# Kernel optimization log

Hardware: AMD Instinct MI355X
Metric: run time of the kernel (lower is better)

## Reference

```python
import jax, jax.numpy as jnp
import numpy as np

B, N, DIM, H, DH, K = 4, 2048, 512, 6, 64, 16
KEEP_PROB = 0.9  # 1 - dropout_rate
LOG2PI = float(np.log(2.0 * np.pi))
LOG_PRIOR = float(np.log(1.0 / K))


def setup_inputs() -> dict:
    key = jax.random.key(0)
    ks = jax.random.split(key, 7)
    inputs_q = jax.random.normal(ks[0], (B, N, DIM), dtype=jnp.float32)
    # decoder-style causal mask, shape [B, 1, q_len, kv_len]
    causal = jnp.tril(jnp.ones((N, N), dtype=jnp.float32))
    mask = jnp.broadcast_to(causal[None, None], (B, 1, N, N))
    # dropout keep mask broadcast across the query dim: [B, H, 1, kv_len]
    keep = jax.random.bernoulli(ks[1], KEEP_PROB, (B, H, 1, N)).astype(jnp.float32)
    w_qkv = jax.random.normal(ks[2], (DIM, 3 * H * DH), dtype=jnp.float32) * 0.02
    w_out = jax.random.normal(ks[3], (H * DH, DIM), dtype=jnp.float32) * 0.02
    mu_lookup = jax.random.normal(ks[4], (K, DIM), dtype=jnp.float32)
    logvar_lookup = jax.random.normal(ks[5], (K, DIM), dtype=jnp.float32) * 0.1
    return {
        "inputs_q": inputs_q,
        "mask": mask,
        "keep": keep,
        "w_qkv": w_qkv,
        "w_out": w_out,
        "mu_lookup": mu_lookup,
        "logvar_lookup": logvar_lookup,
    }


def reference(inputs_q, mask, keep, w_qkv, w_out, mu_lookup, logvar_lookup):
    # --- MultiHeadDotProductAttention (self-attn path) ---
    qkv = (inputs_q @ w_qkv).reshape(B, N, 3, H, DH)  # [B,N,3,H,DH]
    q, k, v = qkv[:, :, 0], qkv[:, :, 1], qkv[:, :, 2]
    # bias: 0 where mask > 0, -1e10 elsewhere (note: no 1/sqrt(d) scaling, as in source)
    bias = jnp.where(mask > 0, 0.0, -1e10)
    attn_weights = jnp.einsum('bqhd,bkhd->bhqk', q, k) + bias  # [B,H,N,N]
    attn_weights = jax.nn.softmax(attn_weights, axis=-1)
    # broadcast dropout: mask shared across the query dim
    attn_weights = attn_weights * keep / KEEP_PROB
    attn_out = jnp.einsum('bhqk,bkhd->bqhd', attn_weights, v)
    attn_out = attn_out.reshape(B, N, H * DH) @ w_out  # [B,N,DIM]

    # --- GMM posterior approx q(y|x) ~= p(y|z) (approx_qy_x, vectorized over k) ---
    z = attn_out.mean(axis=1)  # pooled latent, [B,DIM]
    diff = z[:, None, :] - mu_lookup[None]  # [B,K,DIM]
    llh = -0.5 * jnp.sum(
        diff * diff / jnp.exp(logvar_lookup)[None] + logvar_lookup[None] + LOG2PI,
        axis=-1,
    )  # [B,K]
    logLogit_qy_x = llh + LOG_PRIOR
    qy_x = jax.nn.softmax(logLogit_qy_x, axis=1)  # [B,K]

    # combine mixture mean back in so both branches are live in one output
    return attn_out + (qy_x @ mu_lookup)[:, None, :]
```

## Files before the change

### kernel.cpp

```cpp
#include <hip/hip_runtime.h>
#include <cstdint>
#include <cstddef>

#define NH 6
#define NSEQ 2048
#define DIMD 512
#define BATCH 4
#define HD 384
#define LOG2PI_F 1.8378770664093453f
#define LOG2E_F 1.4426950408889634f
#define M12L2_F (-17.312340490667562f)

typedef __attribute__((ext_vector_type(8))) short short8;
typedef __attribute__((ext_vector_type(8))) unsigned short ushort8;
typedef __attribute__((ext_vector_type(4))) unsigned short ushort4v;
typedef __attribute__((ext_vector_type(4))) float floatx4;

__device__ inline unsigned short f2bf(float f){
  unsigned int u = __float_as_uint(f);
  u += 0x7FFFu + ((u>>16)&1u);
  return (unsigned short)(u>>16);
}

__device__ inline float exp2_raw(float x){
  float r; asm("v_exp_f32 %0, %1" : "=v"(r) : "v"(x)); return r;
}

#define GLD16(gp, lp) __builtin_amdgcn_global_load_lds( \
  (const __attribute__((address_space(1))) void*)(gp), \
  (__attribute__((address_space(3))) void*)(lp), 16, 0, 0)

__device__ inline void wtrans_body(
    const float* __restrict__ src, unsigned short* __restrict__ dst,
    int R, int C, int bx, int by, unsigned short* Ls, int t)
{
  const int r = t>>2, c0 = (t&3)*16;
  const int d0 = by*64, n0 = bx*64;
  #pragma unroll
  for (int j=0;j<16;j+=4){
    floatx4 v = *(const floatx4*)(src + (size_t)(d0+r)*C + n0 + c0 + j);
    #pragma unroll
    for(int jj=0;jj<4;jj++) Ls[r*72 + c0+j+jj] = f2bf(v[jj]);
  }
  __syncthreads();
  #pragma unroll
  for (int j=0;j<16;j+=8){
    ushort8 o;
    #pragma unroll
    for(int jj=0;jj<8;jj++) o[jj] = Ls[(c0+j+jj)*72 + r];
    *(ushort8*)(dst + (size_t)(n0+r)*R + d0 + c0 + j) = o;
  }
}

__global__ __launch_bounds__(256) void prep(
    const float* __restrict__ xq, unsigned short* __restrict__ xbf,
    const float* __restrict__ w_qkv, unsigned short* __restrict__ wqT,
    const float* __restrict__ w_out, unsigned short* __restrict__ woT)
{
  __shared__ __attribute__((aligned(16))) unsigned short Ls[64*72];
  const int bid = blockIdx.x, t = threadIdx.x;
  if (bid < 4096){
    int i = bid*256 + t;
    floatx4 v = *(const floatx4*)(xq + (size_t)i*4);
    ushort4v r;
    #pragma unroll
    for(int j=0;j<4;j++) r[j] = f2bf(v[j]);
    *(ushort4v*)(xbf + (size_t)i*4) = r;
  } else if (bid < 4240){
    int rb = bid - 4096;
    wtrans_body(w_qkv, wqT, 512, 1152, rb%18, rb/18, Ls, t);
  } else {
    int rb = bid - 4240;
    wtrans_body(w_out, woT, 384, 512, rb%8, rb/8, Ls, t);
  }
}

__global__ __launch_bounds__(256) void gemm_qkv(
    const unsigned short* __restrict__ A,
    const unsigned short* __restrict__ Bt,
    const float* __restrict__ keep,
    unsigned short* __restrict__ Qo, unsigned short* __restrict__ Ko,
    unsigned short* __restrict__ Vt)
{
  __shared__ __attribute__((aligned(16))) unsigned short Cs[128*132];
  unsigned short* As = Cs;
  unsigned short* Bs = Cs + 128*64;
  const int tid = threadIdx.x;
  const int w = tid>>6, lane = tid&63;
  const int wr = w>>1, wc = w&1;
  const int quad = lane>>4, l16 = lane&15;
  const int tM = blockIdx.x*128, tN = blockIdx.y*128;
  const int r8 = lane>>3, c8 = (lane&7)*8;
  floatx4 acc[4][4];
  floatx4 zed = {0.f,0.f,0.f,0.f};
  #pragma unroll
  for (int i=0;i<4;i++)
    #pragma unroll
    for(int j=0;j<4;j++) acc[i][j] = zed;

  for (int k0=0; k0<512; k0+=64){
    #pragma unroll
    for (int i=0;i<4;i++){
      int row = w*32 + i*8;
      GLD16(A  + (size_t)(tM+row+r8)*512 + k0 + c8, As + row*64);
      GLD16(Bt + (size_t)(tN+row+r8)*512 + k0 + c8, Bs + row*64);
    }
    __syncthreads();
    #pragma unroll
    for (int kk=0; kk<64; kk+=32){
      short8 af[4], bf[4];
      #pragma unroll
      for(int mt=0;mt<4;mt++)
        af[mt] = *(const short8*)(As + (wr*64+mt*16+l16)*64 + kk + quad*8);
      #pragma unroll
      for(int nt=0;nt<4;nt++)
        bf[nt] = *(const short8*)(Bs + (wc*64+nt*16+l16)*64 + kk + quad*8);
      #pragma unroll
      for(int mt=0;mt<4;mt++)
        #pragma unroll
        for(int nt=0;nt<4;nt++)
          acc[mt][nt] = __builtin_amdgcn_mfma_f32_16x16x32_bf16(af[mt], bf[nt], acc[mt][nt], 0,0,0);
    }
    __syncthreads();
  }
  #pragma unroll
  for(int mt=0;mt<4;mt++)
    #pragma unroll
    for(int nt=0;nt<4;nt++){
      int gcol = tN + wc*64 + nt*16 + l16;
      float qs = (gcol < 384) ? LOG2E_F : 1.0f;
      #pragma unroll
      for(int r=0;r<4;r++)
        Cs[(wr*64+mt*16+quad*4+r)*132 + wc*64+nt*16+l16] = f2bf(acc[mt][nt][r]*qs);
    }
  __syncthreads();
  if (blockIdx.y < 6){
    const int row = tid>>1, colh = (tid&1)*64;
    const int gcol0 = tN + colh;
    const int t = gcol0/384, rem = gcol0 - t*384, h = rem>>6;
    const int grow = tM + row, b = grow>>11, n = grow & 2047;
    unsigned short* dst = (t==0 ? Qo : Ko) + ((size_t)((b*NH+h)*NSEQ+n))*64;
    #pragma unroll
    for(int j=0;j<8;j++)
      *(ushort8*)(dst + j*8) = *(const ushort8*)(Cs + row*132 + colh + j*8);
  } else {
    const int dcol = tid>>1;
    const int nh   = (tid&1)*64;
    const int gcol = tN + dcol;
    const int rem = gcol - 768, h = rem>>6, dh = rem&63;
    const int b = tM>>11, nb = tM & 2047;
    const float* kp = keep + (size_t)(b*NH+h)*NSEQ + nb + nh;
    unsigned short* dst = Vt + ((size_t)((b*NH+h)*64 + dh))*NSEQ + nb + nh;
    #pragma unroll
    for (int j8=0;j8<8;j8++){
      floatx4 k0 = *(const floatx4*)(kp + j8*8);
      floatx4 k1 = *(const floatx4*)(kp + j8*8 + 4);
      ushort8 o;
      #pragma unroll
      for(int u=0;u<4;u++)
        o[u]   = (k0[u] < 0.5f) ? (unsigned short)0 : Cs[(nh + j8*8 + u)*132 + dcol];
      #pragma unroll
      for(int u=0;u<4;u++)
        o[4+u] = (k1[u] < 0.5f) ? (unsigned short)0 : Cs[(nh + j8*8 + 4 + u)*132 + dcol];
      *(ushort8*)(dst + j8*8) = o;
    }
  }
}

__global__ __launch_bounds__(256, 3) void attn_kernel(
    const unsigned short* __restrict__ Qg, const unsigned short* __restrict__ Kg,
    const unsigned short* __restrict__ VtG,
    unsigned short* __restrict__ atp,
    float* __restrict__ zpart)
{
  __shared__ __attribute__((aligned(16))) float sm[4*32*34 + 128];
  float* Ocs  = sm;
  float* accs = sm + 4*32*34;
  const int tid = threadIdx.x;
  const int w = tid>>6, lane = tid&63;
  const int quad = lane>>4, l16 = lane&15;
  const int bid = blockIdx.x;
  const int idx = bid>>3;
  const int bh  = (bid&7) + 8*(idx % 3);
  const int c   = 63 - idx/3;
  const int b = bh/NH, h = bh - b*NH;
  const unsigned short* Qb = Qg  + (size_t)bh*NSEQ*64;
  const int q0 = c*32;
  const int nkt = (c>>1) + 1;
  const int q_abs0 = q0 + l16;

  const unsigned short* Kl = Kg  + (size_t)bh*NSEQ*64 + (size_t)l16*64 + quad*8;
  const unsigned short* Vl = VtG + (size_t)bh*64*NSEQ + (size_t)l16*NSEQ + quad*8;

  short8 qf[2][2];
  #pragma unroll
  for(int mt=0;mt<2;mt++)
    #pragma unroll
    for(int kc=0;kc<2;kc++)
      qf[mt][kc] = *(const short8*)(Qb + (size_t)(q0+mt*16+l16)*64 + kc*32 + quad*8);

  floatx4 O[2][4];
  float accl[2] = {0.f, 0.f};
  floatx4 zed = {0.f,0.f,0.f,0.f};
  floatx4 m12v = {M12L2_F, M12L2_F, M12L2_F, M12L2_F};
  #pragma unroll
  for(int mt=0;mt<2;mt++)
    #pragma unroll
    for(int dt=0;dt<4;dt++) O[mt][dt] = zed;

  for (int kt = w; kt < nkt; kt += 4){
    const int kB = kt*64;
    short8 vf[2][4];
    const unsigned short* vp0 = Vl + kB;
    #pragma unroll
    for(int kh=0;kh<2;kh++)
      #pragma unroll
      for(int dt=0;dt<4;dt++)
        vf[kh][dt] = *(const short8*)(vp0 + (size_t)dt*32768 + kh*32);

    floatx4 sacc[2][4];
    #pragma unroll
    for(int mt=0;mt<2;mt++)
      #pragma unroll
      for(int nt=0;nt<4;nt++) sacc[mt][nt] = m12v;
    const unsigned short* kp0 = Kl + (size_t)kt*4096;
    #pragma unroll
    for(int nt=0;nt<4;nt++){
      short8 kf0 = *(const short8*)(kp0 + nt*1024);
      short8 kf1 = *(const short8*)(kp0 + nt*1024 + 32);
      #pragma unroll
      for(int mt=0;mt<2;mt++){
        sacc[mt][nt] = __builtin_amdgcn_mfma_f32_16x16x32_bf16(kf0, qf[mt][0], sacc[mt][nt], 0,0,0);
        sacc[mt][nt] = __builtin_amdgcn_mfma_f32_16x16x32_bf16(kf1, qf[mt][1], sacc[mt][nt], 0,0,0);
      }
    }

    const bool dia = (kt == nkt-1);
    #pragma unroll
    for(int mt=0;mt<2;mt++){
      const int qa = q_abs0 + mt*16;
      unsigned int d0[4], d1[4];
      float rs = 0.f;
      #pragma unroll
      for(int nt=0;nt<4;nt++){
        const int key0 = kB + nt*16 + quad*4;
        float p0 = exp2_raw(sacc[mt][nt][0]);
        float p1 = exp2_raw(sacc[mt][nt][1]);
        float p2 = exp2_raw(sacc[mt][nt][2]);
        float p3 = exp2_raw(sacc[mt][nt][3]);
        if (dia){
          p0 = (key0   <= qa) ? p0 : 0.f;
          p1 = (key0+1 <= qa) ? p1 : 0.f;
          p2 = (key0+2 <= qa) ? p2 : 0.f;
          p3 = (key0+3 <= qa) ? p3 : 0.f;
        }
        rs += (p0+p1) + (p2+p3);
        asm("v_cvt_pk_bf16_f32 %0, %1, %2" : "=v"(d0[nt]) : "v"(p0), "v"(p1));
        asm("v_cvt_pk_bf16_f32 %0, %1, %2" : "=v"(d1[nt]) : "v"(p2), "v"(p3));
      }
      accl[mt] += rs;
      #pragma unroll
      for(int kh=0;kh<2;kh++){
        unsigned int x0 = d0[2*kh],   x1 = d1[2*kh];
        unsigned int y0 = d0[2*kh+1], y1 = d1[2*kh+1];
        asm("v_permlane32_swap_b32 %0, %1" : "+v"(x0), "+v"(y0));
        asm("v_permlane16_swap_b32 %0, %1" : "+v"(x0), "+v"(y0));
        asm("v_permlane32_swap_b32 %0, %1" : "+v"(x1), "+v"(y1));
        asm("v_permlane16_swap_b32 %0, %1" : "+v"(x1), "+v"(y1));
        union { unsigned int u[4]; short8 s; } cvt;
        cvt.u[0] = x0; cvt.u[1] = x1; cvt.u[2] = y0; cvt.u[3] = y1;
        short8 pf = cvt.s;
        #pragma unroll
        for(int dt=0;dt<4;dt++)
          O[mt][dt] = __builtin_amdgcn_mfma_f32_16x16x32_bf16(pf, vf[kh][dt], O[mt][dt], 0,0,0);
      }
    }
  }

  #pragma unroll
  for(int mt=0;mt<2;mt++){
    accl[mt] += __shfl_xor(accl[mt], 16, 64);
    accl[mt] += __shfl_xor(accl[mt], 32, 64);
  }
  if (quad == 0){
    accs[w*32 + l16]      = accl[0];
    accs[w*32 + 16 + l16] = accl[1];
  }

  const int orow = tid>>3, oc4 = (tid&7)*4;
  float sc2 = 0.f;
  #pragma unroll
  for (int h2=0; h2<2; ++h2){
    float* Ow = Ocs + w*(32*34);
    #pragma unroll
    for(int mt=0;mt<2;mt++)
      #pragma unroll
      for(int d2=0;d2<2;d2++){
        const int dt = h2*2 + d2;
        #pragma unroll
        for(int r=0;r<4;r++)
          Ow[(mt*16+quad*4+r)*34 + d2*16 + l16] = O[mt][dt][r];
      }
    __syncthreads();
    if (h2 == 0){
      float as = accs[orow] + accs[32+orow] + accs[64+orow] + accs[96+orow];
      sc2 = (1.0f/0.9f) / as;
    }
    float fv[4];
    #pragma unroll
    for(int j=0;j<4;j++) fv[j] = 0.f;
    #pragma unroll
    for(int s=0;s<4;s++){
      const float* p = Ocs + s*(32*34) + orow*34 + oc4;
      #pragma unroll
      for(int j=0;j<4;j++) fv[j] += p[j];
    }
    ushort4v o4;
    #pragma unroll
    for(int j=0;j<4;j++){ fv[j] *= sc2; o4[j] = f2bf(fv[j]); }
    *(ushort4v*)(atp + ((size_t)(b*NSEQ + q0 + orow))*HD + h*64 + h2*32 + oc4) = o4;

    #pragma unroll
    for(int j=0;j<4;j++){
      fv[j] += __shfl_xor(fv[j], 8, 64);
      fv[j] += __shfl_xor(fv[j], 16, 64);
      fv[j] += __shfl_xor(fv[j], 32, 64);
    }
    if (lane < 8){
      floatx4 zv; zv[0]=fv[0]; zv[1]=fv[1]; zv[2]=fv[2]; zv[3]=fv[3];
      *(floatx4*)(zpart + ((size_t)(b*256 + c*4 + w))*384 + h*64 + h2*32 + lane*4) = zv;
    }
    __syncthreads();
  }
}

__global__ __launch_bounds__(256) void gmm_kernel(
    const float* __restrict__ zpart,
    const float* __restrict__ wo,
    const float* __restrict__ mu,
    const float* __restrict__ lv, float* __restrict__ c)
{
  __shared__ float zsl[384];
  __shared__ float zl[512];
  __shared__ float sh[16];
  __shared__ float qy[16];
  const int tid = threadIdx.x, b = blockIdx.x;
  for (int e = tid; e < 384; e += 256){
    const float* zp = zpart + (size_t)b*256*384 + e;
    float s0=0.f, s1=0.f, s2=0.f, s3=0.f;
    for (int i=0;i<256;i+=4){
      s0 += zp[(size_t)(i+0)*384];
      s1 += zp[(size_t)(i+1)*384];
      s2 += zp[(size_t)(i+2)*384];
      s3 += zp[(size_t)(i+3)*384];
    }
    zsl[e] = (s0+s1)+(s2+s3);
  }
  __syncthreads();
  #pragma unroll
  for(int dd=0;dd<2;dd++){
    const int d = tid + dd*256;
    float s = 0.f;
    for(int e=0;e<384;e++) s += zsl[e]*wo[(size_t)e*512+d];
    zl[d] = s*(1.0f/2048.0f);
  }
  __syncthreads();
  const int k = tid>>4, li = tid&15;
  float part = 0.f;
  for(int d=li; d<DIMD; d+=16){
    float m = mu[k*DIMD+d], l = lv[k*DIMD+d];
    float diff = zl[d] - m;
    part += diff*diff*__expf(-l) + l + LOG2PI_F;
  }
  #pragma unroll
  for(int off=8;off>=1;off>>=1) part += __shfl_xor(part, off, 64);
  if (li==0) sh[k] = part;
  __syncthreads();
  if (tid<16){
    float logit = -0.5f*sh[tid];
    float mx = logit;
    #pragma unroll
    for(int off=8;off>=1;off>>=1) mx = fmaxf(mx, __shfl_xor(mx, off, 64));
    float e = __expf(logit-mx);
    float se = e;
    #pragma unroll
    for(int off=8;off>=1;off>>=1) se += __shfl_xor(se, off, 64);
    qy[tid] = e/se;
  }
  __syncthreads();
  for(int d=tid; d<DIMD; d+=256){
    float accv = 0.f;
    #pragma unroll
    for(int kk=0;kk<16;kk++) accv += qy[kk]*mu[kk*DIMD+d];
    c[b*DIMD+d] = accv;
  }
}

__global__ __launch_bounds__(256) void gemm_proj(
    const unsigned short* __restrict__ A,
    const unsigned short* __restrict__ Bt,
    const float* __restrict__ cvec,
    float* __restrict__ out)
{
  __shared__ __attribute__((aligned(16))) unsigned short As[128*64];
  __shared__ __attribute__((aligned(16))) unsigned short Bs[128*64];
  const int tid = threadIdx.x;
  const int w = tid>>6, lane = tid&63;
  const int wr = w>>1, wc = w&1;
  const int quad = lane>>4, l16 = lane&15;
  const int tM = blockIdx.x*128, tN = blockIdx.y*128;
  const int r8 = lane>>3, c8 = (lane&7)*8;
  floatx4 acc[4][4];
  floatx4 zed = {0.f,0.f,0.f,0.f};
  #pragma unroll
  for (int i=0;i<4;i++)
    #pragma unroll
    for(int j=0;j<4;j++) acc[i][j] = zed;

  for (int k0=0; k0<384; k0+=64){
    #pragma unroll
    for (int i=0;i<4;i++){
      int row = w*32 + i*8;
      GLD16(A  + (size_t)(tM+row+r8)*384 + k0 + c8, As + row*64);
      GLD16(Bt + (size_t)(tN+row+r8)*384 + k0 + c8, Bs + row*64);
    }
    __syncthreads();
    #pragma unroll
    for (int kk=0; kk<64; kk+=32){
      short8 af[4], bf[4];
      #pragma unroll
      for(int mt=0;mt<4;mt++)
        af[mt] = *(const short8*)(As + (wr*64+mt*16+l16)*64 + kk + quad*8);
      #pragma unroll
      for(int nt=0;nt<4;nt++)
        bf[nt] = *(const short8*)(Bs + (wc*64+nt*16+l16)*64 + kk + quad*8);
      #pragma unroll
      for(int mt=0;mt<4;mt++)
        #pragma unroll
        for(int nt=0;nt<4;nt++)
          acc[mt][nt] = __builtin_amdgcn_mfma_f32_16x16x32_bf16(af[mt], bf[nt], acc[mt][nt], 0,0,0);
    }
    __syncthreads();
  }
  const int bq = tM>>11;
  #pragma unroll
  for(int nt=0;nt<4;nt++){
    const int gcol = tN + wc*64 + nt*16 + l16;
    const float cc = cvec[bq*DIMD + gcol];
    #pragma unroll
    for(int mt=0;mt<4;mt++){
      const int grow = tM + wr*64 + mt*16 + quad*4;
      #pragma unroll
      for(int r=0;r<4;r++)
        out[(size_t)(grow+r)*512 + gcol] = acc[mt][nt][r] + cc;
    }
  }
}

extern "C" void kernel_launch(void* const* d_in, const int* in_sizes, int n_in,
                              void* d_out, int out_size, void* d_ws, size_t ws_size,
                              hipStream_t stream) {
  const float* inputs_q = (const float*)d_in[0];
  const float* keep  = (const float*)d_in[2];
  const float* w_qkv = (const float*)d_in[3];
  const float* w_out = (const float*)d_in[4];
  const float* mu    = (const float*)d_in[5];
  const float* lv    = (const float*)d_in[6];
  float* out = (float*)d_out;
  char* ws = (char*)d_ws;
  size_t off = 0;
  auto alloc = [&](size_t bytes){ void* p = ws + off; off += (bytes + 255) & ~(size_t)255; return p; };
  unsigned short* Qb  = (unsigned short*)alloc((size_t)24*2048*64*2);
  unsigned short* Kb  = (unsigned short*)alloc((size_t)24*2048*64*2);
  unsigned short* Vt  = (unsigned short*)alloc((size_t)24*64*2048*2);
  unsigned short* xbf = (unsigned short*)alloc((size_t)8192*512*2);
  unsigned short* wqT = (unsigned short*)alloc((size_t)1152*512*2);
  unsigned short* woT = (unsigned short*)alloc((size_t)512*384*2);
  unsigned short* atp = (unsigned short*)alloc((size_t)8192*384*2);
  float* zpart = (float*)alloc((size_t)4*256*384*4);
  float* c     = (float*)alloc((size_t)4*512*4);

  prep<<<4288, 256, 0, stream>>>(inputs_q, xbf, w_qkv, wqT, w_out, woT);
  gemm_qkv<<<dim3(64,9), 256, 0, stream>>>(xbf, wqT, keep, Qb, Kb, Vt);
  attn_kernel<<<1536, 256, 0, stream>>>(Qb, Kb, Vt, atp, zpart);
  gmm_kernel<<<4, 256, 0, stream>>>(zpart, w_out, mu, lv, c);
  gemm_proj<<<dim3(64,4), 256, 0, stream>>>(atp, woT, c, out);
}
```

Baseline: 253.3 us.

## Parallelize pooled-latent reduction in a separate wide kernel with transposed partials

```diff
diff --git a/kernel.cpp b/kernel.cpp
--- a/kernel.cpp
+++ b/kernel.cpp
@@ -327,15 +327,31 @@
       fv[j] += __shfl_xor(fv[j], 32, 64);
     }
     if (lane < 8){
-      floatx4 zv; zv[0]=fv[0]; zv[1]=fv[1]; zv[2]=fv[2]; zv[3]=fv[3];
-      *(floatx4*)(zpart + ((size_t)(b*256 + c*4 + w))*384 + h*64 + h2*32 + lane*4) = zv;
-    }
-    __syncthreads();
-  }
+      float* zp = zpart + ((size_t)(b*HD + h*64 + h2*32 + lane*4))*256 + c*4 + w;
+      zp[0]     = fv[0];
+      zp[256]   = fv[1];
+      zp[512]   = fv[2];
+      zp[768]   = fv[3];
+    }
+    __syncthreads();
+  }
+}
+
+__global__ __launch_bounds__(256) void zred(
+    const float* __restrict__ zpart,
+    float* __restrict__ zsum)
+{
+  const int o = blockIdx.x*4 + (threadIdx.x>>6);
+  const int lane = threadIdx.x & 63;
+  floatx4 v = *(const floatx4*)(zpart + (size_t)o*256 + lane*4);
+  float s = (v[0]+v[1]) + (v[2]+v[3]);
+  #pragma unroll
+  for(int off=32;off>=1;off>>=1) s += __shfl_xor(s, off, 64);
+  if (lane == 0) zsum[o] = s;
 }
 
 __global__ __launch_bounds__(256) void gmm_kernel(
-    const float* __restrict__ zpart,
+    const float* __restrict__ zsum,
     const float* __restrict__ wo,
     const float* __restrict__ mu,
     const float* __restrict__ lv, float* __restrict__ c)
@@ -345,17 +361,7 @@
   __shared__ float sh[16];
   __shared__ float qy[16];
   const int tid = threadIdx.x, b = blockIdx.x;
-  for (int e = tid; e < 384; e += 256){
-    const float* zp = zpart + (size_t)b*256*384 + e;
-    float s0=0.f, s1=0.f, s2=0.f, s3=0.f;
-    for (int i=0;i<256;i+=4){
-      s0 += zp[(size_t)(i+0)*384];
-      s1 += zp[(size_t)(i+1)*384];
-      s2 += zp[(size_t)(i+2)*384];
-      s3 += zp[(size_t)(i+3)*384];
-    }
-    zsl[e] = (s0+s1)+(s2+s3);
-  }
+  for (int e = tid; e < 384; e += 256) zsl[e] = zsum[(size_t)b*HD + e];
   __syncthreads();
   #pragma unroll
   for(int dd=0;dd<2;dd++){
@@ -477,12 +483,14 @@
   unsigned short* wqT = (unsigned short*)alloc((size_t)1152*512*2);
   unsigned short* woT = (unsigned short*)alloc((size_t)512*384*2);
   unsigned short* atp = (unsigned short*)alloc((size_t)8192*384*2);
-  float* zpart = (float*)alloc((size_t)4*256*384*4);
+  float* zpart = (float*)alloc((size_t)4*384*256*4);
+  float* zsum  = (float*)alloc((size_t)4*384*4);
   float* c     = (float*)alloc((size_t)4*512*4);
 
   prep<<<4288, 256, 0, stream>>>(inputs_q, xbf, w_qkv, wqT, w_out, woT);
   gemm_qkv<<<dim3(64,9), 256, 0, stream>>>(xbf, wqT, keep, Qb, Kb, Vt);
   attn_kernel<<<1536, 256, 0, stream>>>(Qb, Kb, Vt, atp, zpart);
-  gmm_kernel<<<4, 256, 0, stream>>>(zpart, w_out, mu, lv, c);
+  zred<<<384, 256, 0, stream>>>(zpart, zsum);
+  gmm_kernel<<<4, 256, 0, stream>>>(zsum, w_out, mu, lv, c);
   gemm_proj<<<dim3(64,4), 256, 0, stream>>>(atp, woT, c, out);
 }
```

Result: faster. 246.0 us (-2.9%).
